# Optimization experiments

Measured on AMD Instinct MI355X. Metric: run time of the kernel, lower is better.

Reference implementation:

```python
import jax, jax.numpy as jnp
import numpy as np

E = 800000
N = 50000
D = 128
SLOPE = 0.2


def setup_inputs() -> dict:
    key = jax.random.key(0)
    ks = jax.random.split(key, 8)
    M = jax.random.normal(ks[0], (E, D), dtype=jnp.float32)
    dest = jax.random.randint(ks[1], (E,), 0, N, dtype=jnp.int32)
    rev_index = jax.random.randint(ks[2], (E,), 0, E, dtype=jnp.int32)
    s = 1.0 / np.sqrt(D)
    W0 = jax.random.uniform(ks[3], (D, D), jnp.float32, -s, s)
    b0 = jax.random.uniform(ks[4], (D,), jnp.float32, -s, s)
    W1 = jax.random.uniform(ks[5], (D, D), jnp.float32, -s, s)
    b1 = jax.random.uniform(ks[6], (D,), jnp.float32, -s, s)
    sa = 1.0 / np.sqrt(D)
    a_w = jax.random.uniform(ks[7], (1, D), jnp.float32, -sa, sa)
    a_b = jnp.zeros((1,), jnp.float32)
    return {"M": M, "dest": dest, "rev_index": rev_index, "dim_size": N,
            "W0": W0, "b0": b0, "W1": W1, "b1": b1, "a_w": a_w, "a_b": a_b}


def reference(M, dest, rev_index, dim_size, W0, b0, W1, b1, a_w, a_b):
    # Z = LeakyReLU(W_0(M) + W_1(M[rev_index]))  -> [E, D]
    Z = jax.nn.leaky_relu(M @ W0.T + b0 + M[rev_index] @ W1.T + b1, negative_slope=SLOPE)
    # scores = a(Z) -> [E, 1]; segment softmax over dest
    s = (Z @ a_w.T + a_b)[:, 0]  # [E]
    smax = jax.ops.segment_max(s, dest, num_segments=dim_size)  # [N]
    e = jnp.exp(s - smax[dest])
    denom = jax.ops.segment_sum(e, dest, num_segments=dim_size)  # [N]
    alpha = (e / denom[dest])[:, None]  # [E, 1]
    out = jax.ops.segment_sum(alpha * M, dest, num_segments=dim_size)  # [N, D]
    return out, alpha
```

## Files before the change

kernel.cpp:

```cpp
#include <hip/hip_runtime.h>
#include <hip/hip_bf16.h>


#define SLOPE 0.2f
constexpr int E = 800000;
constexpr int N = 50000;
constexpr int D = 128;
constexpr int TILE_E = 64;
constexpr int NTILES = E / TILE_E;
constexpr int LDA = 264;
constexpr int MAXDEG = 64;

typedef __attribute__((ext_vector_type(8))) short bf16x8;
typedef __attribute__((ext_vector_type(4))) short short4v;
typedef __attribute__((ext_vector_type(4))) float f32x4;

__device__ __forceinline__ short f2bf(float f) {
    unsigned u = __float_as_uint(f);
    u = (u + 0x7fffu + ((u >> 16) & 1u)) >> 16;
    return (short)u;
}

__global__ void convert_w(const float* __restrict__ W0, const float* __restrict__ W1,
                          short* __restrict__ Wbf) {
    int i = blockIdx.x * blockDim.x + threadIdx.x;
    if (i >= D * 256) return;
    int d = i >> 8, k = i & 255;
    float v = (k < 128) ? W0[d * 128 + k] : W1[d * 128 + (k - 128)];
    Wbf[i] = f2bf(v);
}

__global__ void bucket_build(const int* __restrict__ dest, int* __restrict__ cnt,
                             int* __restrict__ bucket) {
    int e = blockIdx.x * blockDim.x + threadIdx.x;
    if (e >= E) return;
    int n = dest[e];
    int pos = atomicAdd(&cnt[n], 1);
    if (pos < MAXDEG) bucket[n * MAXDEG + pos] = e;
}

__global__ __launch_bounds__(512) void score_kernel(
    const float* __restrict__ M, const int* __restrict__ dest,
    const int* __restrict__ rev, const short* __restrict__ Wbf,
    const float* __restrict__ b0, const float* __restrict__ b1,
    const float* __restrict__ a_w, const float* __restrict__ a_b,
    float* __restrict__ pbuf, float* __restrict__ denom)
{
    __shared__ short Alds[TILE_E * LDA];
    __shared__ float red[4][TILE_E];

    const int t = threadIdx.x;
    const int w = t >> 6;
    const int lane = t & 63;
    const int lo = lane & 15, hi = lane >> 4;
    const int er = (w & 1) * 32;
    const int dr = (w >> 1) * 32;

    bf16x8 b[2][8];
#pragma unroll
    for (int j = 0; j < 2; ++j) {
        int d = dr + j * 16 + lo;
#pragma unroll
        for (int ks = 0; ks < 8; ++ks)
            b[j][ks] = *(const bf16x8*)(Wbf + d * 256 + ks * 32 + hi * 8);
    }
    float bs[2], aw[2];
#pragma unroll
    for (int j = 0; j < 2; ++j) {
        int d = dr + j * 16 + lo;
        bs[j] = b0[d] + b1[d];
        aw[j] = a_w[d];
    }
    const float ab = a_b[0];

    const int c  = t & 31;
    const int r0 = t >> 5;

    for (int tile = blockIdx.x; tile < NTILES; tile += gridDim.x) {
        const int ebase = tile * TILE_E;
        __syncthreads();

#pragma unroll
        for (int pp = 0; pp < 2; ++pp) {
            float4 vs[2], vr[2];
            int rv[2];
#pragma unroll
            for (int q = 0; q < 2; ++q)
                rv[q] = rev[ebase + r0 + (pp * 2 + q) * 16];
#pragma unroll
            for (int q = 0; q < 2; ++q)
                vs[q] = ((const float4*)(M + (size_t)(ebase + r0 + (pp * 2 + q) * 16) * D))[c];
#pragma unroll
            for (int q = 0; q < 2; ++q)
                vr[q] = ((const float4*)(M + (size_t)rv[q] * D))[c];
#pragma unroll
            for (int q = 0; q < 2; ++q) {
                int r = r0 + (pp * 2 + q) * 16;
                short4v s0 = { f2bf(vs[q].x), f2bf(vs[q].y), f2bf(vs[q].z), f2bf(vs[q].w) };
                *(short4v*)(Alds + r * LDA + c * 4) = s0;
                short4v s1 = { f2bf(vr[q].x), f2bf(vr[q].y), f2bf(vr[q].z), f2bf(vr[q].w) };
                *(short4v*)(Alds + r * LDA + 128 + c * 4) = s1;
            }
        }
        __syncthreads();

        f32x4 zero = {0.f, 0.f, 0.f, 0.f};
        f32x4 acc[2][2];
#pragma unroll
        for (int i = 0; i < 2; ++i)
#pragma unroll
            for (int j = 0; j < 2; ++j) acc[i][j] = zero;

#pragma unroll
        for (int ks = 0; ks < 8; ++ks) {
            bf16x8 a[2];
#pragma unroll
            for (int i = 0; i < 2; ++i)
                a[i] = *(const bf16x8*)(Alds + (er + i * 16 + lo) * LDA + ks * 32 + hi * 8);
#pragma unroll
            for (int i = 0; i < 2; ++i)
#pragma unroll
                for (int j = 0; j < 2; ++j)
                    acc[i][j] = __builtin_amdgcn_mfma_f32_16x16x32_bf16(a[i], b[j][ks], acc[i][j], 0, 0, 0);
        }

#pragma unroll
        for (int i = 0; i < 2; ++i) {
#pragma unroll
            for (int r = 0; r < 4; ++r) {
                float v = 0.f;
#pragma unroll
                for (int j = 0; j < 2; ++j) {
                    float x = acc[i][j][r] + bs[j];
                    x = (x > 0.f) ? x : SLOPE * x;
                    v += aw[j] * x;
                }
                v += __shfl_xor(v, 1);
                v += __shfl_xor(v, 2);
                v += __shfl_xor(v, 4);
                v += __shfl_xor(v, 8);
                if (lo == 0) red[w >> 1][er + i * 16 + hi * 4 + r] = v;
            }
        }
        __syncthreads();

        if (t < TILE_E) {
            float s = red[0][t] + red[1][t] + red[2][t] + red[3][t] + ab;
            float p = __expf(s);
            pbuf[ebase + t] = p;
            atomicAdd(&denom[dest[ebase + t]], p);
        }
    }
}

__global__ void norm_kernel(const int* __restrict__ dest, const float* __restrict__ denom,
                            float* __restrict__ alpha) {
    int e = blockIdx.x * blockDim.x + threadIdx.x;
    if (e < E) alpha[e] = alpha[e] / denom[dest[e]];
}

__global__ __launch_bounds__(256) void gather_kernel(
    const float* __restrict__ M, const float* __restrict__ alpha,
    const int* __restrict__ cnt, const int* __restrict__ bucket,
    float* __restrict__ out)
{
    const int n = blockIdx.x * 4 + (threadIdx.x >> 6);
    const int lane = threadIdx.x & 63;
    int c = cnt[n];
    c = (c > MAXDEG) ? MAXDEG : c;
    int e = 0; float a = 0.f;
    if (lane < c) {
        e = bucket[n * MAXDEG + lane];
        a = alpha[e];
    }
    float2 acc = {0.f, 0.f};
    for (int i = 0; i < c; ++i) {
        int   ei = __shfl(e, i);
        float ai = __shfl(a, i);
        float2 v = ((const float2*)(M + (size_t)ei * D))[lane];
        acc.x += ai * v.x;
        acc.y += ai * v.y;
    }
    ((float2*)(out + (size_t)n * D))[lane] = acc;
}

extern "C" void kernel_launch(void* const* d_in, const int* in_sizes, int n_in,
                              void* d_out, int out_size, void* d_ws, size_t ws_size,
                              hipStream_t stream) {
    const float* M   = (const float*)d_in[0];
    const int*   dst = (const int*)d_in[1];
    const int*   rev = (const int*)d_in[2];
    const float* W0  = (const float*)d_in[4];
    const float* b0  = (const float*)d_in[5];
    const float* W1  = (const float*)d_in[6];
    const float* b1  = (const float*)d_in[7];
    const float* a_w = (const float*)d_in[8];
    const float* a_b = (const float*)d_in[9];

    float* out   = (float*)d_out;
    float* alpha = out + (size_t)N * D;

    float* denom  = (float*)d_ws;
    short* Wbf    = (short*)(denom + N);
    int*   cnt    = (int*)(Wbf + D * 256);
    int*   bucket = cnt + N;

    hipMemsetAsync(denom, 0, (size_t)N * sizeof(float), stream);
    hipMemsetAsync(cnt, 0, (size_t)N * sizeof(int), stream);

    convert_w<<<128, 256, 0, stream>>>(W0, W1, Wbf);
    bucket_build<<<(E + 255) / 256, 256, 0, stream>>>(dst, cnt, bucket);
    score_kernel<<<512, 512, 0, stream>>>(M, dst, rev, Wbf, b0, b1, a_w, a_b, alpha, denom);
    norm_kernel<<<(E + 255) / 256, 256, 0, stream>>>(dst, denom, alpha);
    gather_kernel<<<N / 4, 256, 0, stream>>>(M, alpha, cnt, bucket, out);
}
```

Baseline: 765.2 us.

## Fuse alpha normalization into gather kernel and unroll gather loop

```diff
diff --git a/kernel.cpp b/kernel.cpp
--- a/kernel.cpp
+++ b/kernel.cpp
@@ -39,7 +39,7 @@
     if (pos < MAXDEG) bucket[n * MAXDEG + pos] = e;
 }
 
-__global__ __launch_bounds__(512) void score_kernel(
+__global__ __launch_bounds__(512, 4) void score_kernel(
     const float* __restrict__ M, const int* __restrict__ dest,
     const int* __restrict__ rev, const short* __restrict__ Wbf,
     const float* __restrict__ b0, const float* __restrict__ b1,
@@ -153,14 +153,9 @@
     }
 }
 
-__global__ void norm_kernel(const int* __restrict__ dest, const float* __restrict__ denom,
-                            float* __restrict__ alpha) {
-    int e = blockIdx.x * blockDim.x + threadIdx.x;
-    if (e < E) alpha[e] = alpha[e] / denom[dest[e]];
-}
-
 __global__ __launch_bounds__(256) void gather_kernel(
-    const float* __restrict__ M, const float* __restrict__ alpha,
+    const float* __restrict__ M, float* __restrict__ alpha,
+    const float* __restrict__ denom,
     const int* __restrict__ cnt, const int* __restrict__ bucket,
     float* __restrict__ out)
 {
@@ -168,18 +163,35 @@
     const int lane = threadIdx.x & 63;
     int c = cnt[n];
     c = (c > MAXDEG) ? MAXDEG : c;
+    const float dn = denom[n];
     int e = 0; float a = 0.f;
     if (lane < c) {
         e = bucket[n * MAXDEG + lane];
-        a = alpha[e];
+        a = alpha[e] / dn;
+        alpha[e] = a;
     }
     float2 acc = {0.f, 0.f};
-    for (int i = 0; i < c; ++i) {
+    int i = 0;
+    for (; i + 4 <= c; i += 4) {
+        int   e0 = __shfl(e, i + 0), e1 = __shfl(e, i + 1),
+              e2 = __shfl(e, i + 2), e3 = __shfl(e, i + 3);
+        float a0 = __shfl(a, i + 0), a1 = __shfl(a, i + 1),
+              a2 = __shfl(a, i + 2), a3 = __shfl(a, i + 3);
+        float2 v0 = ((const float2*)(M + (size_t)e0 * D))[lane];
+        float2 v1 = ((const float2*)(M + (size_t)e1 * D))[lane];
+        float2 v2 = ((const float2*)(M + (size_t)e2 * D))[lane];
+        float2 v3 = ((const float2*)(M + (size_t)e3 * D))[lane];
+        acc.x = fmaf(a0, v0.x, acc.x); acc.y = fmaf(a0, v0.y, acc.y);
+        acc.x = fmaf(a1, v1.x, acc.x); acc.y = fmaf(a1, v1.y, acc.y);
+        acc.x = fmaf(a2, v2.x, acc.x); acc.y = fmaf(a2, v2.y, acc.y);
+        acc.x = fmaf(a3, v3.x, acc.x); acc.y = fmaf(a3, v3.y, acc.y);
+    }
+    for (; i < c; ++i) {
         int   ei = __shfl(e, i);
         float ai = __shfl(a, i);
         float2 v = ((const float2*)(M + (size_t)ei * D))[lane];
-        acc.x += ai * v.x;
-        acc.y += ai * v.y;
+        acc.x = fmaf(ai, v.x, acc.x);
+        acc.y = fmaf(ai, v.y, acc.y);
     }
     ((float2*)(out + (size_t)n * D))[lane] = acc;
 }
@@ -211,6 +223,5 @@
     convert_w<<<128, 256, 0, stream>>>(W0, W1, Wbf);
     bucket_build<<<(E + 255) / 256, 256, 0, stream>>>(dst, cnt, bucket);
     score_kernel<<<512, 512, 0, stream>>>(M, dst, rev, Wbf, b0, b1, a_w, a_b, alpha, denom);
-    norm_kernel<<<(E + 255) / 256, 256, 0, stream>>>(dst, denom, alpha);
-    gather_kernel<<<N / 4, 256, 0, stream>>>(M, alpha, cnt, bucket, out);
-}
+    gather_kernel<<<N / 4, 256, 0, stream>>>(M, alpha, denom, cnt, bucket, out);
+}
```

Result: no change. 751.6 us (-1.8%).
